# Optimization experiments

Hardware: AMD Instinct MI355X
Metric: run time of the kernel (lower is better)

## Reference

```python
import jax, jax.numpy as jnp
import numpy as np

EPS = 1e-8


def setup_inputs() -> dict:
    key = jax.random.key(0)
    k1, k2, k3, k4, k5 = jax.random.split(key, 5)
    N, B, T, D = 8, 2, 2048, 2048
    F = 4 * D
    blocks = jax.random.normal(k1, (N, B, T, D), dtype=jnp.float32)
    partial_block = jax.random.normal(k2, (B, T, D), dtype=jnp.float32)
    proj_w = jax.random.normal(k3, (D,), dtype=jnp.float32) * 0.02
    norm_scale = jnp.ones((D,), dtype=jnp.float32)
    ffn_w1 = jax.random.normal(k4, (D, F), dtype=jnp.float32) * 0.02
    ffn_w2 = jax.random.normal(k5, (F, D), dtype=jnp.float32) * 0.02
    return {
        "blocks": blocks,
        "partial_block": partial_block,
        "proj_w": proj_w,
        "norm_scale": norm_scale,
        "ffn_w1": ffn_w1,
        "ffn_w2": ffn_w2,
    }


def reference(blocks, partial_block, proj_w, norm_scale, ffn_w1, ffn_w2):
    # Stack completed blocks with current partial sum: V [N1, B, T, D]
    V = jnp.concatenate([blocks, partial_block[None]], axis=0)
    # RMSNorm over D (keys)
    rms = jnp.sqrt(jnp.mean(V * V, axis=-1, keepdims=True) + EPS)
    K = norm_scale * V / rms
    # Pseudo-query dot-product logits [N1, B, T], softmax over blocks (axis 0)
    logits = jnp.einsum('nbtd,d->nbt', K, proj_w)
    alpha = jax.nn.softmax(logits, axis=0)
    # Weighted sum of raw values -> new hidden state h [B, T, D]
    h = jnp.einsum('nbt,nbtd->btd', alpha, V)
    # Sublayer: standard FFN (D -> 4D gelu -> D)
    f_out = jax.nn.gelu(h @ ffn_w1) @ ffn_w2
    # layer_number % block_size != 0 branch: accumulate partial sum
    new_partial = partial_block + f_out
    return h, new_partial
```

## Files before the change

kernel.cpp:

```cpp
#include <hip/hip_runtime.h>

typedef unsigned short ushort_t;
typedef __bf16 bf16x8 __attribute__((ext_vector_type(8)));
typedef float f32x4 __attribute__((ext_vector_type(4)));

#define NB 8
#define BB 2
#define TT 2048
#define DD 2048
#define FF 8192
#define MM (BB * TT)
#define BTD ((size_t)BB * TT * DD)

__device__ __forceinline__ unsigned short f2bf(float f) {
  unsigned int u = __float_as_uint(f);
  u += 0x7FFFu + ((u >> 16) & 1u);
  return (unsigned short)(u >> 16);
}

__device__ __forceinline__ float gelu_tanh(float x) {
  float u = 0.7978845608028654f * (x + 0.044715f * x * x * x);
  float e = __expf(2.0f * u);
  float th = 1.0f - 2.0f / (e + 1.0f);
  return 0.5f * x * (1.0f + th);
}

template <int N>
__device__ __forceinline__ void wait_vmcnt() {
  if constexpr (N == 0) asm volatile("s_waitcnt vmcnt(0)" ::: "memory");
  else if constexpr (N == 8) asm volatile("s_waitcnt vmcnt(8)" ::: "memory");
  else if constexpr (N == 10) asm volatile("s_waitcnt vmcnt(10)" ::: "memory");
}

#define ASYNC_COPY16(gp, lp)                                                   \
  __builtin_amdgcn_global_load_lds(                                            \
      (__attribute__((address_space(1))) void*)(gp),                           \
      (__attribute__((address_space(3))) void*)(lp), 16, 0, 0)

__global__ __launch_bounds__(256) void transpose_conv(
    const float* __restrict__ in, ushort_t* __restrict__ out, int R, int C) {
  __shared__ float tile[32][33];
  const int tx = threadIdx.x & 31, ty = threadIdx.x >> 5;
  const int r0 = blockIdx.y * 32, c0 = blockIdx.x * 32;
#pragma unroll
  for (int i = 0; i < 32; i += 8)
    tile[ty + i][tx] = in[(size_t)(r0 + ty + i) * C + (c0 + tx)];
  __syncthreads();
#pragma unroll
  for (int i = 0; i < 32; i += 8)
    out[(size_t)(c0 + ty + i) * R + (r0 + tx)] = f2bf(tile[tx][ty + i]);
}

__global__ __launch_bounds__(256) void attn_fuse(
    const float* __restrict__ blocks, const float* __restrict__ partial,
    const float* __restrict__ proj_w, const float* __restrict__ norm_scale,
    float* __restrict__ h_out, ushort_t* __restrict__ h_bf) {
  const int t = threadIdx.x;
  const int bt = blockIdx.x;
  const size_t rowoff = (size_t)bt * DD;
  const int d0 = t * 4;

  float w[8];
  {
    float4 ns = *(const float4*)(norm_scale + d0);
    float4 pw = *(const float4*)(proj_w + d0);
    w[0] = ns.x * pw.x; w[1] = ns.y * pw.y; w[2] = ns.z * pw.z; w[3] = ns.w * pw.w;
    ns = *(const float4*)(norm_scale + 1024 + d0);
    pw = *(const float4*)(proj_w + 1024 + d0);
    w[4] = ns.x * pw.x; w[5] = ns.y * pw.y; w[6] = ns.z * pw.z; w[7] = ns.w * pw.w;
  }

  float vv[9][8];
  float ss[9], dt[9];
#pragma unroll
  for (int n = 0; n < 9; ++n) {
    const float* rp = (n < 8) ? (blocks + (size_t)n * BTD + rowoff)
                              : (partial + rowoff);
    float4 v0 = *(const float4*)(rp + d0);
    float4 v1 = *(const float4*)(rp + 1024 + d0);
    vv[n][0] = v0.x; vv[n][1] = v0.y; vv[n][2] = v0.z; vv[n][3] = v0.w;
    vv[n][4] = v1.x; vv[n][5] = v1.y; vv[n][6] = v1.z; vv[n][7] = v1.w;
    float a = 0.f, c = 0.f;
#pragma unroll
    for (int j = 0; j < 8; ++j) {
      a += vv[n][j] * vv[n][j];
      c += vv[n][j] * w[j];
    }
    ss[n] = a; dt[n] = c;
  }

  __shared__ float red[2][9][4];
  const int lane = t & 63, wv = t >> 6;
#pragma unroll
  for (int n = 0; n < 9; ++n) {
    float a = ss[n], c = dt[n];
#pragma unroll
    for (int off = 32; off > 0; off >>= 1) {
      a += __shfl_down(a, off, 64);
      c += __shfl_down(c, off, 64);
    }
    if (lane == 0) { red[0][n][wv] = a; red[1][n][wv] = c; }
  }
  __syncthreads();
  __shared__ float logit_s[9];
  if (t < 9) {
    float a = red[0][t][0] + red[0][t][1] + red[0][t][2] + red[0][t][3];
    float c = red[1][t][0] + red[1][t][1] + red[1][t][2] + red[1][t][3];
    logit_s[t] = c * rsqrtf(a * (1.0f / (float)DD) + 1e-8f);
  }
  __syncthreads();

  float lg[9], mx = -1e30f;
#pragma unroll
  for (int n = 0; n < 9; ++n) { lg[n] = logit_s[n]; mx = fmaxf(mx, lg[n]); }
  float den = 0.0f;
#pragma unroll
  for (int n = 0; n < 9; ++n) { lg[n] = __expf(lg[n] - mx); den += lg[n]; }
  const float inv = 1.0f / den;

  float h[8] = {0, 0, 0, 0, 0, 0, 0, 0};
#pragma unroll
  for (int n = 0; n < 9; ++n) {
    const float a = lg[n] * inv;
#pragma unroll
    for (int j = 0; j < 8; ++j) h[j] += a * vv[n][j];
  }

  float4 o0 = {h[0], h[1], h[2], h[3]}, o1 = {h[4], h[5], h[6], h[7]};
  *(float4*)(h_out + rowoff + d0) = o0;
  *(float4*)(h_out + rowoff + 1024 + d0) = o1;
  uint2 p0, p1;
  p0.x = (unsigned)f2bf(h[0]) | ((unsigned)f2bf(h[1]) << 16);
  p0.y = (unsigned)f2bf(h[2]) | ((unsigned)f2bf(h[3]) << 16);
  p1.x = (unsigned)f2bf(h[4]) | ((unsigned)f2bf(h[5]) << 16);
  p1.y = (unsigned)f2bf(h[6]) | ((unsigned)f2bf(h[7]) << 16);
  *(uint2*)(h_bf + rowoff + d0) = p0;
  *(uint2*)(h_bf + rowoff + 1024 + d0) = p1;
}

template <int BN, int EPI>
__global__ __launch_bounds__(512, 2) void gemm256(
    const ushort_t* __restrict__ A, const ushort_t* __restrict__ BT,
    const int K, const int N, const int GX, ushort_t* __restrict__ Cb,
    const float* __restrict__ addend, float* __restrict__ Cf) {
  constexpr int BM = 256;
  constexpr int WCN = BN / 4;
  constexpr int MF = 8;
  constexpr int NF = WCN / 16;
  constexpr int NH = NF / 2;
  constexpr int NCB = BN / 64;
  constexpr int AUS = BM * 64;
  constexpr int WP = (BN == 256) ? 10 : 8;

  __shared__ __align__(16) ushort_t lds0[(BM + BN) * 64];
  __shared__ __align__(16) ushort_t lds1[(BM + BN) * 64];

  const int t = threadIdx.x;
  const int lane = t & 63, wv = t >> 6;
  const int wr = wv >> 2, wc = wv & 3;
  const int fr = lane & 15;

  const int nwg = gridDim.x;
  const int wg = blockIdx.x;
  const int swz = (wg & 7) * (nwg >> 3) + (wg >> 3);
  const int bx = swz % GX, by = swz / GX;
  const int row0 = by * BM, col0 = bx * BN;

  const int sr = t >> 3;
  const int scolb = ((t & 7) * 16) ^ ((sr & 7) << 4);
  const ushort_t* gA = A + (size_t)(row0 + sr) * K + (scolb >> 1);
  const ushort_t* gB = BT + (size_t)(col0 + sr) * K + (scolb >> 1);

#define ST_A(W, c, KT)                                                         \
  ASYNC_COPY16(gA + (size_t)((c)*64) * K + (KT)*64, &W[(c)*4096 + wv * 512])
#define ST_B(W, c, KT)                                                         \
  ASYNC_COPY16(gB + (size_t)((c)*64) * K + (KT)*64,                            \
               &W[AUS + (c)*4096 + wv * 512])
#define STAGE_BALL(W, KT)                                                      \
  { _Pragma("unroll") for (int _c = 0; _c < NCB; ++_c) ST_B(W, _c, KT); }

  const int s_lane = (fr & 7) << 4;
  const int offk0 = ((lane >> 4) * 16) ^ s_lane;
  const int offk1 = (64 + (lane >> 4) * 16) ^ s_lane;
  const int aoffA = (wr * 128 + fr) * 128;
  int boffB[NF];
#pragma unroll
  for (int n = 0; n < NF; ++n)
    boffB[n] = AUS * 2 + (wc * WCN + n * 16 + fr) * 128;

  bf16x8 af[4][2], b0[NH][2], b1[NH][2];

#define READ_A(Lb, MO)                                                         \
  _Pragma("unroll") for (int m = 0; m < 4; ++m) {                              \
    af[m][0] =                                                                 \
        *(const bf16x8*)((const char*)(Lb) + aoffA + (MO + m) * 2048 + offk0); \
    af[m][1] =                                                                 \
        *(const bf16x8*)((const char*)(Lb) + aoffA + (MO + m) * 2048 + offk1); \
  }
#define READ_B(Lb, DST, NO)                                                    \
  _Pragma("unroll") for (int n = 0; n < NH; ++n) {                             \
    DST[n][0] = *(const bf16x8*)((const char*)(Lb) + boffB[NO + n] + offk0);   \
    DST[n][1] = *(const bf16x8*)((const char*)(Lb) + boffB[NO + n] + offk1);   \
  }

  f32x4 acc[MF][NF];
#pragma unroll
  for (int m = 0; m < MF; ++m)
#pragma unroll
    for (int n = 0; n < NF; ++n) {
      f32x4 z = {0.f, 0.f, 0.f, 0.f};
      acc[m][n] = z;
    }

#define MFMA_(a, b, c) __builtin_amdgcn_mfma_f32_16x16x32_bf16(a, b, c, 0, 0, 0)
#define QUAD(BF, MO, NO)                                                       \
  _Pragma("unroll") for (int ks = 0; ks < 2; ++ks)                             \
    _Pragma("unroll") for (int m = 0; m < 4; ++m)                              \
      _Pragma("unroll") for (int n = 0; n < NH; ++n)                           \
        acc[MO + m][NO + n] =                                                  \
            MFMA_(af[m][ks], BF[n][ks], acc[MO + m][NO + n]);

#define HALF(Rb, KT)                                                           \
  {                                                                            \
    const bool _s = (KT) + 2 < NT;                                             \
                                                   \
    READ_B(Rb, b0, 0);                                                         \
    READ_A(Rb, 0);                                                             \
    __builtin_amdgcn_sched_barrier(0);                                         \
    __builtin_amdgcn_s_barrier();                                              \
    __builtin_amdgcn_s_setprio(1);                                             \
    QUAD(b0, 0, 0);                                                            \
    __builtin_amdgcn_s_setprio(0);                                             \
    __builtin_amdgcn_s_barrier();                                              \
                                        \
    READ_B(Rb, b1, NH);                                                        \
    if (_s) { ST_A(Rb, 0, (KT) + 2); ST_A(Rb, 2, (KT) + 2); }                  \
    __builtin_amdgcn_sched_barrier(0);                                         \
    __builtin_amdgcn_s_barrier();                                              \
    __builtin_amdgcn_s_setprio(1);                                             \
    QUAD(b1, 0, NH);                                                           \
    __builtin_amdgcn_s_setprio(0);                                             \
    wait_vmcnt<WP>();                                                          \
    __builtin_amdgcn_s_barrier();                                              \
                                         \
    READ_A(Rb, 4);                                                             \
    if (_s) STAGE_BALL(Rb, (KT) + 2);                                          \
    __builtin_amdgcn_sched_barrier(0);                                         \
    __builtin_amdgcn_s_barrier();                                              \
    __builtin_amdgcn_s_setprio(1);                                             \
    QUAD(b1, 4, NH);                                                           \
    __builtin_amdgcn_s_setprio(0);                                             \
    __builtin_amdgcn_s_barrier();                                              \
                                   \
    if (_s) { ST_A(Rb, 1, (KT) + 2); ST_A(Rb, 3, (KT) + 2); }                  \
    __builtin_amdgcn_sched_barrier(0);                                         \
    __builtin_amdgcn_s_barrier();                                              \
    __builtin_amdgcn_s_setprio(1);                                             \
    QUAD(b0, 4, 0);                                                            \
    __builtin_amdgcn_s_setprio(0);                                             \
    wait_vmcnt<WP>();                                                          \
    __builtin_amdgcn_s_barrier();                                              \
  }

  const int NT = K >> 6;

  ST_A(lds0, 0, 0); ST_A(lds0, 2, 0);
  STAGE_BALL(lds0, 0);
  ST_A(lds0, 1, 0); ST_A(lds0, 3, 0);
  ST_A(lds1, 0, 1); ST_A(lds1, 2, 1);
  STAGE_BALL(lds1, 1);
  ST_A(lds1, 1, 1); ST_A(lds1, 3, 1);
  wait_vmcnt<WP>();
  __builtin_amdgcn_s_barrier();

  for (int kt = 0; kt < NT; kt += 2) {
    HALF(lds0, kt);
    HALF(lds1, kt + 1);
  }

  const int r4 = (lane >> 4) * 4;
#pragma unroll
  for (int m = 0; m < MF; ++m) {
    const int grow = row0 + wr * 128 + m * 16 + r4;
#pragma unroll
    for (int n = 0; n < NF; ++n) {
      const int gcol = col0 + wc * WCN + n * 16 + fr;
#pragma unroll
      for (int r = 0; r < 4; ++r) {
        const float v = acc[m][n][r];
        const size_t idx = (size_t)(grow + r) * N + gcol;
        if (EPI == 0) {
          Cb[idx] = f2bf(gelu_tanh(v));
        } else {
          Cf[idx] = v + addend[idx];
        }
      }
    }
  }
#undef HALF
#undef QUAD
#undef MFMA_
#undef READ_A
#undef READ_B
#undef STAGE_BALL
#undef ST_A
#undef ST_B
}

extern "C" void kernel_launch(void* const* d_in, const int* in_sizes, int n_in,
                              void* d_out, int out_size, void* d_ws,
                              size_t ws_size, hipStream_t stream) {
  const float* blocks = (const float*)d_in[0];
  const float* partial = (const float*)d_in[1];
  const float* proj_w = (const float*)d_in[2];
  const float* norm_scale = (const float*)d_in[3];
  const float* w1 = (const float*)d_in[4];
  const float* w2 = (const float*)d_in[5];

  float* out = (float*)d_out;
  float* h_out = out;
  float* new_partial = out + BTD;

  char* ws = (char*)d_ws;
  ushort_t* h_bf = (ushort_t*)ws;
  ushort_t* w1T = (ushort_t*)(ws + (size_t)16777216);
  ushort_t* w2T = (ushort_t*)(ws + (size_t)16777216 + 33554432);
  ushort_t* act = (ushort_t*)(ws + (size_t)16777216 + 2 * 33554432ull);

  transpose_conv<<<dim3(FF / 32, DD / 32), 256, 0, stream>>>(w1, w1T, DD, FF);
  transpose_conv<<<dim3(DD / 32, FF / 32), 256, 0, stream>>>(w2, w2T, FF, DD);

  attn_fuse<<<MM, 256, 0, stream>>>(blocks, partial, proj_w, norm_scale, h_out,
                                    h_bf);

  gemm256<256, 0><<<(FF / 256) * (MM / 256), 512, 0, stream>>>(
      h_bf, w1T, DD, FF, FF / 256, act, nullptr, nullptr);
  gemm256<128, 1><<<(DD / 128) * (MM / 256), 512, 0, stream>>>(
      act, w2T, FF, DD, DD / 128, nullptr, partial, new_partial);
}
```

Measured before the change: 433.7 us.

## Restructure GEMM prefetch into 8-phase cross-buffer pipeline with XCD-aware tile mapping

```diff
diff --git a/kernel.cpp b/kernel.cpp
--- a/kernel.cpp
+++ b/kernel.cpp
@@ -28,8 +28,8 @@
 template <int N>
 __device__ __forceinline__ void wait_vmcnt() {
   if constexpr (N == 0) asm volatile("s_waitcnt vmcnt(0)" ::: "memory");
-  else if constexpr (N == 8) asm volatile("s_waitcnt vmcnt(8)" ::: "memory");
-  else if constexpr (N == 10) asm volatile("s_waitcnt vmcnt(10)" ::: "memory");
+  else if constexpr (N == 2) asm volatile("s_waitcnt vmcnt(2)" ::: "memory");
+  else if constexpr (N == 4) asm volatile("s_waitcnt vmcnt(4)" ::: "memory");
 }
 
 #define ASYNC_COPY16(gp, lp)                                                   \
@@ -138,33 +138,31 @@
   *(uint2*)(h_bf + rowoff + 1024 + d0) = p1;
 }
 
-template <int BN, int EPI>
-__global__ __launch_bounds__(512, 2) void gemm256(
+template <int BN, int EPI, int SBY, int SBX, int MCX>
+__global__ __launch_bounds__(512, 2) void gemm8(
     const ushort_t* __restrict__ A, const ushort_t* __restrict__ BT,
-    const int K, const int N, const int GX, ushort_t* __restrict__ Cb,
+    const int K, const int N, ushort_t* __restrict__ Cb,
     const float* __restrict__ addend, float* __restrict__ Cf) {
-  constexpr int BM = 256;
   constexpr int WCN = BN / 4;
-  constexpr int MF = 8;
-  constexpr int NF = WCN / 16;
-  constexpr int NH = NF / 2;
+  constexpr int NFR = WCN / 16;
+  constexpr int NH = NFR / 2;
   constexpr int NCB = BN / 64;
-  constexpr int AUS = BM * 64;
-  constexpr int WP = (BN == 256) ? 10 : 8;
-
-  __shared__ __align__(16) ushort_t lds0[(BM + BN) * 64];
-  __shared__ __align__(16) ushort_t lds1[(BM + BN) * 64];
+  constexpr int AUS = 256 * 64;
+  constexpr int VMC = (BN == 256) ? 4 : 2;
+
+  __shared__ __align__(16) ushort_t lds0[(256 + BN) * 64];
+  __shared__ __align__(16) ushort_t lds1[(256 + BN) * 64];
 
   const int t = threadIdx.x;
   const int lane = t & 63, wv = t >> 6;
   const int wr = wv >> 2, wc = wv & 3;
   const int fr = lane & 15;
 
-  const int nwg = gridDim.x;
   const int wg = blockIdx.x;
-  const int swz = (wg & 7) * (nwg >> 3) + (wg >> 3);
-  const int bx = swz % GX, by = swz / GX;
-  const int row0 = by * BM, col0 = bx * BN;
+  const int xcd = wg & 7, local = wg >> 3;
+  const int by = (xcd / MCX) * SBY + local / SBX;
+  const int bx = (xcd % MCX) * SBX + local % SBX;
+  const int row0 = by * 256, col0 = bx * BN;
 
   const int sr = t >> 3;
   const int scolb = ((t & 7) * 16) ^ ((sr & 7) << 4);
@@ -176,19 +174,17 @@
 #define ST_B(W, c, KT)                                                         \
   ASYNC_COPY16(gB + (size_t)((c)*64) * K + (KT)*64,                            \
                &W[AUS + (c)*4096 + wv * 512])
-#define STAGE_BALL(W, KT)                                                      \
-  { _Pragma("unroll") for (int _c = 0; _c < NCB; ++_c) ST_B(W, _c, KT); }
 
   const int s_lane = (fr & 7) << 4;
   const int offk0 = ((lane >> 4) * 16) ^ s_lane;
   const int offk1 = (64 + (lane >> 4) * 16) ^ s_lane;
   const int aoffA = (wr * 128 + fr) * 128;
-  int boffB[NF];
-#pragma unroll
-  for (int n = 0; n < NF; ++n)
+  int boffB[NFR];
+#pragma unroll
+  for (int n = 0; n < NFR; ++n)
     boffB[n] = AUS * 2 + (wc * WCN + n * 16 + fr) * 128;
 
-  bf16x8 af[4][2], b0[NH][2], b1[NH][2];
+  bf16x8 af[4][2], bn0[NH][2], bn1[NH][2];
 
 #define READ_A(Lb, MO)                                                         \
   _Pragma("unroll") for (int m = 0; m < 4; ++m) {                              \
@@ -203,11 +199,11 @@
     DST[n][1] = *(const bf16x8*)((const char*)(Lb) + boffB[NO + n] + offk1);   \
   }
 
-  f32x4 acc[MF][NF];
-#pragma unroll
-  for (int m = 0; m < MF; ++m)
-#pragma unroll
-    for (int n = 0; n < NF; ++n) {
+  f32x4 acc[8][NFR];
+#pragma unroll
+  for (int m = 0; m < 8; ++m)
+#pragma unroll
+    for (int n = 0; n < NFR; ++n) {
       f32x4 z = {0.f, 0.f, 0.f, 0.f};
       acc[m][n] = z;
     }
@@ -220,70 +216,69 @@
         acc[MO + m][NO + n] =                                                  \
             MFMA_(af[m][ks], BF[n][ks], acc[MO + m][NO + n]);
 
-#define HALF(Rb, KT)                                                           \
+#define BAR __builtin_amdgcn_s_barrier()
+#define PRIO1 __builtin_amdgcn_s_setprio(1)
+#define PRIO0 __builtin_amdgcn_s_setprio(0)
+
+#define ITER(X, Y, a)                                                          \
   {                                                                            \
-    const bool _s = (KT) + 2 < NT;                                             \
-                                                   \
-    READ_B(Rb, b0, 0);                                                         \
-    READ_A(Rb, 0);                                                             \
-    __builtin_amdgcn_sched_barrier(0);                                         \
-    __builtin_amdgcn_s_barrier();                                              \
-    __builtin_amdgcn_s_setprio(1);                                             \
-    QUAD(b0, 0, 0);                                                            \
-    __builtin_amdgcn_s_setprio(0);                                             \
-    __builtin_amdgcn_s_barrier();                                              \
-                                        \
-    READ_B(Rb, b1, NH);                                                        \
-    if (_s) { ST_A(Rb, 0, (KT) + 2); ST_A(Rb, 2, (KT) + 2); }                  \
-    __builtin_amdgcn_sched_barrier(0);                                         \
-    __builtin_amdgcn_s_barrier();                                              \
-    __builtin_amdgcn_s_setprio(1);                                             \
-    QUAD(b1, 0, NH);                                                           \
-    __builtin_amdgcn_s_setprio(0);                                             \
-    wait_vmcnt<WP>();                                                          \
-    __builtin_amdgcn_s_barrier();                                              \
-                                         \
-    READ_A(Rb, 4);                                                             \
-    if (_s) STAGE_BALL(Rb, (KT) + 2);                                          \
-    __builtin_amdgcn_sched_barrier(0);                                         \
-    __builtin_amdgcn_s_barrier();                                              \
-    __builtin_amdgcn_s_setprio(1);                                             \
-    QUAD(b1, 4, NH);                                                           \
-    __builtin_amdgcn_s_setprio(0);                                             \
-    __builtin_amdgcn_s_barrier();                                              \
-                                   \
-    if (_s) { ST_A(Rb, 1, (KT) + 2); ST_A(Rb, 3, (KT) + 2); }                  \
-    __builtin_amdgcn_sched_barrier(0);                                         \
-    __builtin_amdgcn_s_barrier();                                              \
-    __builtin_amdgcn_s_setprio(1);                                             \
-    QUAD(b0, 4, 0);                                                            \
-    __builtin_amdgcn_s_setprio(0);                                             \
-    wait_vmcnt<WP>();                                                          \
-    __builtin_amdgcn_s_barrier();                                              \
+    const bool s2 = (a) + 2 < NT, s3 = (a) + 3 < NT;                           \
+                 \
+    READ_B(X, bn0, 0);                                                         \
+    READ_A(X, 0);                                                              \
+    ST_A(Y, 0, (a) + 1); ST_A(Y, 1, (a) + 1);                                  \
+    BAR; PRIO1; QUAD(bn0, 0, 0); PRIO0; BAR;                                   \
+                           \
+    READ_B(X, bn1, NH);                                                        \
+    ST_A(Y, 2, (a) + 1); ST_A(Y, 3, (a) + 1);                                  \
+    BAR; PRIO1; QUAD(bn1, 0, NH); PRIO0; BAR;                                  \
+                           \
+    READ_A(X, 4);                                                              \
+    if (s2) { ST_B(X, 0, (a) + 2); ST_B(X, 1, (a) + 2); }                      \
+    BAR; PRIO1; QUAD(bn1, 4, NH); PRIO0; BAR;                                  \
+                     \
+    if (s2 && NCB == 4) { ST_B(X, 2, (a) + 2); ST_B(X, 3, (a) + 2); }          \
+    BAR; PRIO1; QUAD(bn0, 4, 0); PRIO0;                                        \
+    if (s2) wait_vmcnt<VMC>(); else wait_vmcnt<0>();                           \
+    BAR;                                                                       \
+                 \
+    READ_B(Y, bn0, 0);                                                         \
+    READ_A(Y, 0);                                                              \
+    if (s2) { ST_A(X, 0, (a) + 2); ST_A(X, 1, (a) + 2); }                      \
+    BAR; PRIO1; QUAD(bn0, 0, 0); PRIO0; BAR;                                   \
+                           \
+    READ_B(Y, bn1, NH);                                                        \
+    if (s2) { ST_A(X, 2, (a) + 2); ST_A(X, 3, (a) + 2); }                      \
+    BAR; PRIO1; QUAD(bn1, 0, NH); PRIO0; BAR;                                  \
+                           \
+    READ_A(Y, 4);                                                              \
+    if (s3) { ST_B(Y, 0, (a) + 3); ST_B(Y, 1, (a) + 3); }                      \
+    BAR; PRIO1; QUAD(bn1, 4, NH); PRIO0; BAR;                                  \
+                     \
+    if (s3 && NCB == 4) { ST_B(Y, 2, (a) + 3); ST_B(Y, 3, (a) + 3); }          \
+    BAR; PRIO1; QUAD(bn0, 4, 0); PRIO0;                                        \
+    if (s2) wait_vmcnt<VMC>(); else wait_vmcnt<0>();                           \
+    BAR;                                                                       \
   }
 
   const int NT = K >> 6;
 
-  ST_A(lds0, 0, 0); ST_A(lds0, 2, 0);
-  STAGE_BALL(lds0, 0);
-  ST_A(lds0, 1, 0); ST_A(lds0, 3, 0);
-  ST_A(lds1, 0, 1); ST_A(lds1, 2, 1);
-  STAGE_BALL(lds1, 1);
-  ST_A(lds1, 1, 1); ST_A(lds1, 3, 1);
-  wait_vmcnt<WP>();
+#pragma unroll
+  for (int c = 0; c < NCB; ++c) ST_B(lds0, c, 0);
+  ST_A(lds0, 0, 0); ST_A(lds0, 1, 0); ST_A(lds0, 2, 0); ST_A(lds0, 3, 0);
+#pragma unroll
+  for (int c = 0; c < NCB; ++c) ST_B(lds1, c, 1);
+  wait_vmcnt<VMC>();
   __builtin_amdgcn_s_barrier();
 
-  for (int kt = 0; kt < NT; kt += 2) {
-    HALF(lds0, kt);
-    HALF(lds1, kt + 1);
-  }
+  for (int a = 0; a < NT; a += 2) ITER(lds0, lds1, a);
 
   const int r4 = (lane >> 4) * 4;
 #pragma unroll
-  for (int m = 0; m < MF; ++m) {
+  for (int m = 0; m < 8; ++m) {
     const int grow = row0 + wr * 128 + m * 16 + r4;
 #pragma unroll
-    for (int n = 0; n < NF; ++n) {
+    for (int n = 0; n < NFR; ++n) {
       const int gcol = col0 + wc * WCN + n * 16 + fr;
 #pragma unroll
       for (int r = 0; r < 4; ++r) {
@@ -297,12 +292,14 @@
       }
     }
   }
-#undef HALF
+#undef ITER
+#undef BAR
+#undef PRIO1
+#undef PRIO0
 #undef QUAD
 #undef MFMA_
 #undef READ_A
 #undef READ_B
-#undef STAGE_BALL
 #undef ST_A
 #undef ST_B
 }
@@ -333,8 +330,8 @@
   attn_fuse<<<MM, 256, 0, stream>>>(blocks, partial, proj_w, norm_scale, h_out,
                                     h_bf);
 
-  gemm256<256, 0><<<(FF / 256) * (MM / 256), 512, 0, stream>>>(
-      h_bf, w1T, DD, FF, FF / 256, act, nullptr, nullptr);
-  gemm256<128, 1><<<(DD / 128) * (MM / 256), 512, 0, stream>>>(
-      act, w2T, FF, DD, DD / 128, nullptr, partial, new_partial);
-}
+  gemm8<256, 0, 8, 8, 4><<<512, 512, 0, stream>>>(
+      h_bf, w1T, DD, FF, act, nullptr, nullptr);
+  gemm8<128, 1, 4, 8, 2><<<256, 512, 0, stream>>>(
+      act, w2T, FF, DD, nullptr, partial, new_partial);
+}
```

Result: faster. 421.2 us (-2.9%).
